# Kernel optimization log

Hardware: AMD Instinct MI355X
Metric: run time of the kernel (lower is better)

The kernel has to match this reference:

```python
import jax, jax.numpy as jnp
import numpy as np

B, S, D, DH, H, HD, F, L = 32, 4096, 256, 128, 8, 32, 64, 4
EPS_BN, EPS_LN = 1e-5, 1e-5


def _conv1d(x, w, b, pad):
    # x: [B,C,S], w: [O,I,K] (torch layout)
    y = jax.lax.conv_general_dilated(x, w, (1,), [(pad, pad)],
                                     dimension_numbers=('NCH', 'OIH', 'NCH'))
    return y + b[None, :, None]


def _bn_eval(x, g, b):
    # BatchNorm1d in eval mode with running_mean=0, running_var=1 (fresh init)
    return x * (g / jnp.sqrt(1.0 + EPS_BN))[None, :, None] + b[None, :, None]


def _ln(x, g, b):
    m = x.mean(-1, keepdims=True)
    v = ((x - m) ** 2).mean(-1, keepdims=True)
    return (x - m) / jnp.sqrt(v + EPS_LN) * g + b


def _gelu(x):
    return jax.nn.gelu(x, approximate=False)


def _pos_encoding(seq_len, d_model):
    pos = jnp.arange(seq_len, dtype=jnp.float32)[:, None]
    div = jnp.exp(jnp.arange(0, d_model, 2, dtype=jnp.float32) * (-np.log(10000.0) / d_model))
    pe = jnp.zeros((seq_len, d_model), jnp.float32)
    pe = pe.at[:, 0::2].set(jnp.sin(pos * div))
    pe = pe.at[:, 1::2].set(jnp.cos(pos * div))
    return pe


def _performer_attn(x, wq, bq, wk, bk, wv, bv, wo, bo, rf):
    b_, s_, d_ = x.shape
    def heads(y):
        return y.reshape(b_, s_, H, HD).transpose(0, 2, 1, 3)  # [B,H,S,hd]
    q, k, v = heads(x @ wq + bq), heads(x @ wk + bk), heads(x @ wv + bv)
    qp = jax.nn.softplus(jnp.einsum('bhsd,hdf->bhsf', q, rf))
    kp = jax.nn.softplus(jnp.einsum('bhsd,hdf->bhsf', k, rf))
    kv = jnp.einsum('bhsf,bhsd->bhfd', kp, v)          # [B,H,F,hd]
    ksum = kp.sum(axis=2)                              # [B,H,F]
    qkv = jnp.einsum('bhsf,bhfd->bhsd', qp, kv)
    denom = jnp.einsum('bhsf,bhf->bhs', qp, ksum) + 1e-8
    out = (qkv / denom[..., None]).transpose(0, 2, 1, 3).reshape(b_, s_, d_)
    return out @ wo + bo


def _forward(x, emb_w1, emb_b1, bn1_g, bn1_b, emb_w2, emb_b2, bn2_g, bn2_b,
             wq, bq, wk, bk, wv, bv, wo, bo, rf,
             ln1_g, ln1_b, ln2_g, ln2_b, ff_w1, ff_b1, ff_w2, ff_b2,
             dec_w1, dec_b1, bn3_g, bn3_b, dec_w2, dec_b2):
    h = _gelu(_bn_eval(_conv1d(x[:, None, :], emb_w1, emb_b1, 3), bn1_g, bn1_b))
    h = _gelu(_bn_eval(_conv1d(h, emb_w2, emb_b2, 2), bn2_g, bn2_b))
    h = h.transpose(0, 2, 1)                           # [B,S,D]
    h = h + _pos_encoding(h.shape[1], h.shape[2])[None]
    for i in range(L):
        a = _performer_attn(_ln(h, ln1_g[i], ln1_b[i]),
                            wq[i], bq[i], wk[i], bk[i], wv[i], bv[i], wo[i], bo[i], rf[i])
        h = h + a
        f = _ln(h, ln2_g[i], ln2_b[i])
        f = _gelu(f @ ff_w1[i] + ff_b1[i]) @ ff_w2[i] + ff_b2[i]
        h = h + f
    hc = h.transpose(0, 2, 1)
    hc = _gelu(_bn_eval(_conv1d(hc, dec_w1, dec_b1, 2), bn3_g, bn3_b))
    hc = _conv1d(hc, dec_w2, dec_b2, 1)
    return jax.nn.sigmoid(hc)[:, 0, :]                 # [B,S]


def setup_inputs() -> dict:
    key = jax.random.key(0)
    ks = iter(jax.random.split(key, 64))
    def rn(shape, s=1.0):
        return jax.random.normal(next(ks), shape, jnp.float32) * s
    return {
        'x': rn((B, S)),
        'emb_w1': rn((DH, 1, 7), 0.3), 'emb_b1': rn((DH,), 0.02),
        'bn1_g': 1.0 + rn((DH,), 0.02), 'bn1_b': rn((DH,), 0.02),
        'emb_w2': rn((D, DH, 5), 0.05), 'emb_b2': rn((D,), 0.02),
        'bn2_g': 1.0 + rn((D,), 0.02), 'bn2_b': rn((D,), 0.02),
        'wq': rn((L, D, D), 0.05), 'bq': rn((L, D), 0.02),
        'wk': rn((L, D, D), 0.05), 'bk': rn((L, D), 0.02),
        'wv': rn((L, D, D), 0.05), 'bv': rn((L, D), 0.02),
        'wo': rn((L, D, D), 0.05), 'bo': rn((L, D), 0.02),
        'rf': rn((L, H, HD, F), 1.0 / np.sqrt(F)),
        'ln1_g': jnp.ones((L, D)), 'ln1_b': jnp.zeros((L, D)),
        'ln2_g': jnp.ones((L, D)), 'ln2_b': jnp.zeros((L, D)),
        'ff_w1': rn((L, D, 4 * D), 0.05), 'ff_b1': rn((L, 4 * D), 0.02),
        'ff_w2': rn((L, 4 * D, D), 0.03), 'ff_b2': rn((L, D), 0.02),
        'dec_w1': rn((DH, D, 5), 0.05), 'dec_b1': rn((DH,), 0.02),
        'bn3_g': 1.0 + rn((DH,), 0.02), 'bn3_b': rn((DH,), 0.02),
        'dec_w2': rn((1, DH, 3), 0.1), 'dec_b2': rn((1,), 0.02),
    }


def reference(x, emb_w1, emb_b1, bn1_g, bn1_b, emb_w2, emb_b2, bn2_g, bn2_b,
              wq, bq, wk, bk, wv, bv, wo, bo, rf,
              ln1_g, ln1_b, ln2_g, ln2_b, ff_w1, ff_b1, ff_w2, ff_b2,
              dec_w1, dec_b1, bn3_g, bn3_b, dec_w2, dec_b2):
    return _forward(x, emb_w1, emb_b1, bn1_g, bn1_b, emb_w2, emb_b2, bn2_g, bn2_b,
                    wq, bq, wk, bk, wv, bv, wo, bo, rf,
                    ln1_g, ln1_b, ln2_g, ln2_b, ff_w1, ff_b1, ff_w2, ff_b2,
                    dec_w1, dec_b1, bn3_g, bn3_b, dec_w2, dec_b2)
```

## Files before the change

kernel.cpp:

```cpp
#include <hip/hip_runtime.h>
#include <hip/hip_bf16.h>
#include <math.h>


typedef __bf16 bf16_t;
typedef __bf16 bf16x8 __attribute__((ext_vector_type(8)));
typedef __bf16 bf16x4 __attribute__((ext_vector_type(4)));
typedef float  f32x4  __attribute__((ext_vector_type(4)));

#define DEV __device__ __forceinline__

DEV float erf_fast(float x) {
  float ax = fabsf(x);
  float t = __builtin_amdgcn_rcpf(1.f + 0.3275911f * ax);
  float p = t * (0.254829592f + t * (-0.284496736f + t * (1.421413741f +
            t * (-1.453152027f + t * 1.061405429f))));
  float r = 1.f - p * __expf(-ax * ax);
  return copysignf(r, x);
}
DEV float geluf(float v) { return 0.5f * v * (1.f + erf_fast(v * 0.70710678118654752440f)); }
DEV float softplusf(float v) {
  float e = __expf(-fabsf(v));
  return fmaxf(v, 0.f) + __logf(1.f + e);
}

DEV void gload16(const bf16_t* g, bf16_t* l) {
  __builtin_amdgcn_global_load_lds(
      (const __attribute__((address_space(1))) void*)g,
      (__attribute__((address_space(3))) void*)l, 16, 0, 0);
}

template <int EPI, int K>
__global__ __launch_bounds__(256, 3)
void gemm_bf16(const bf16_t* __restrict__ A, const bf16_t* __restrict__ Bt,
               void* Cout, const float* __restrict__ bias,
               const float* __restrict__ scale, const float* resid,
               const float* __restrict__ pe,
               int lda, long a_bstride, int rpb,
               int N, int ldc, long c_bstride, int c_roff)
{
  __shared__ bf16_t As[3][128 * 32];
  __shared__ bf16_t Bs[3][128 * 32];
  const int t = threadIdx.x;
  const int lane = t & 63;
  const int w = t >> 6;
  const int wm = w >> 1, wn = w & 1;
  const long m0 = (long)blockIdx.x * 128;
  const int n0 = blockIdx.y * 128;
  const int b = (int)(m0 / rpb);
  const int s_base = (int)(m0 % rpb);
  const bf16_t* Ab = A + (long)b * a_bstride + (long)s_base * lda;
  const bf16_t* Bb = Bt + (long)n0 * K;

  const int srow = lane >> 2;
  const int sslot = (lane & 3) ^ ((srow >> 1) & 3);
  const bf16_t* aS = Ab + (long)(w * 32 + srow) * lda + sslot * 8;
  const bf16_t* bS = Bb + (long)(w * 32 + srow) * K + sslot * 8;
  const int dsto = w * 1024;

#define STAGE(bufidx, kk)                                   \
  {                                                         \
    bf16_t* a_ = &As[bufidx][dsto];                         \
    bf16_t* b_ = &Bs[bufidx][dsto];                         \
    gload16(aS + (kk), a_);                                 \
    gload16(aS + (kk) + 16 * (long)lda, a_ + 512);          \
    gload16(bS + (kk), b_);                                 \
    gload16(bS + (kk) + 16 * (long)K, b_ + 512);            \
  }

  f32x4 acc[4][4];
#pragma unroll
  for (int i = 0; i < 4; i++)
#pragma unroll
    for (int j = 0; j < 4; j++) acc[i][j] = (f32x4){0.f, 0.f, 0.f, 0.f};

  constexpr int NT = K >> 5;
  STAGE(0, 0);
  STAGE(1, 32);

#pragma unroll
  for (int tt = 0; tt < NT; ++tt) {
    if (tt + 1 < NT) {
      asm volatile("s_waitcnt vmcnt(4)" ::: "memory");
    } else {
      asm volatile("s_waitcnt vmcnt(0)" ::: "memory");
    }
    __builtin_amdgcn_s_barrier();
    __builtin_amdgcn_sched_barrier(0);
    if (tt + 2 < NT) STAGE((tt + 2) % 3, (tt + 2) * 32);
    const int cb = tt % 3;
    const bf16_t* Acur = As[cb];
    const bf16_t* Bcur = Bs[cb];
    const int kb = (lane >> 4) * 16;
    bf16x8 af[4], bfr[4];
#pragma unroll
    for (int i = 0; i < 4; i++) {
      int rA = wm * 64 + i * 16 + (lane & 15);
      af[i] = *(const bf16x8*)((const char*)Acur + rA * 64 + (kb ^ (((rA >> 1) & 3) << 4)));
      int rB = wn * 64 + i * 16 + (lane & 15);
      bfr[i] = *(const bf16x8*)((const char*)Bcur + rB * 64 + (kb ^ (((rB >> 1) & 3) << 4)));
    }
    __builtin_amdgcn_s_setprio(1);
#pragma unroll
    for (int mi = 0; mi < 4; mi++)
#pragma unroll
      for (int ni = 0; ni < 4; ni++)
        acc[mi][ni] = __builtin_amdgcn_mfma_f32_16x16x32_bf16(af[mi], bfr[ni], acc[mi][ni], 0, 0, 0);
    __builtin_amdgcn_s_setprio(0);
  }
#undef STAGE

  const int colbase = n0 + wn * 64 + (lane & 15);
  float bias_r[4], scale_r[4];
#pragma unroll
  for (int ni = 0; ni < 4; ni++) {
    int col = colbase + ni * 16;
    bias_r[ni] = bias[col];
    scale_r[ni] = (EPI == 3 || EPI == 4) ? scale[col] : 0.f;
  }
#pragma unroll
  for (int mi = 0; mi < 4; mi++) {
#pragma unroll
    for (int j = 0; j < 4; j++) {
      int row = wm * 64 + mi * 16 + ((lane >> 4) << 2) + j;
      long s = s_base + row;
      long cro = (long)b * c_bstride + (s + c_roff) * (long)ldc;
#pragma unroll
      for (int ni = 0; ni < 4; ni++) {
        int col = colbase + ni * 16;
        float v = acc[mi][ni][j];
        if constexpr (EPI == 1) {
          v += bias_r[ni] + resid[cro + col];
          ((float*)Cout)[cro + col] = v;
        } else if constexpr (EPI == 2) {
          v = geluf(v + bias_r[ni]);
          ((bf16_t*)Cout)[cro + col] = (bf16_t)v;
        } else if constexpr (EPI == 3) {
          v = geluf(v * scale_r[ni] + bias_r[ni]) + pe[s * 256 + col];
          ((float*)Cout)[cro + col] = v;
        } else if constexpr (EPI == 4) {
          v = geluf(v * scale_r[ni] + bias_r[ni]);
          ((bf16_t*)Cout)[cro + col] = (bf16_t)v;
        } else {
          v += bias_r[ni];
          if (col < 1024) v = softplusf(v);
          ((bf16_t*)Cout)[cro + col] = (bf16_t)v;
        }
      }
    }
  }
}

__global__ __launch_bounds__(256)
void ln_kernel(const float* __restrict__ h, const float* __restrict__ g,
               const float* __restrict__ bta, bf16_t* __restrict__ out)
{
  int t = threadIdx.x;
  int lane = t & 63;
  long row = (long)blockIdx.x * 4 + (t >> 6);
  const float* hp = h + row * 256 + lane * 4;
  float4 v = *(const float4*)hp;
  float s = v.x + v.y + v.z + v.w;
  float q = v.x * v.x + v.y * v.y + v.z * v.z + v.w * v.w;
#pragma unroll
  for (int m = 32; m >= 1; m >>= 1) {
    s += __shfl_xor(s, m);
    q += __shfl_xor(q, m);
  }
  float mean = s * 0.00390625f;
  float var = q * 0.00390625f - mean * mean;
  float rstd = rsqrtf(var + 1e-5f);
  int c = lane * 4;
  float4 gv = *(const float4*)(g + c);
  float4 bv = *(const float4*)(bta + c);
  bf16x4 o;
  o[0] = (bf16_t)((v.x - mean) * rstd * gv.x + bv.x);
  o[1] = (bf16_t)((v.y - mean) * rstd * gv.y + bv.y);
  o[2] = (bf16_t)((v.z - mean) * rstd * gv.z + bv.z);
  o[3] = (bf16_t)((v.w - mean) * rstd * gv.w + bv.w);
  *(bf16x4*)(out + row * 256 + c) = o;
}

__global__ __launch_bounds__(256)
void conv1_kernel(const float* __restrict__ x, const float* __restrict__ w1,
                  const float* __restrict__ sc, const float* __restrict__ sb,
                  bf16_t* __restrict__ h1p)
{
  int b = blockIdx.x >> 6;
  int s0 = (blockIdx.x & 63) << 6;
  __shared__ float xs[70];
  __shared__ float ws[896];
  int t = threadIdx.x;
  if (t < 70) {
    int s = s0 + t - 3;
    xs[t] = (s >= 0 && s < 4096) ? x[(long)b * 4096 + s] : 0.f;
  }
  for (int i = t; i < 896; i += 256) ws[i] = w1[i];
  __syncthreads();
  int c = t & 127, so = t >> 7;
  float wr[7];
#pragma unroll
  for (int k = 0; k < 7; k++) wr[k] = ws[c * 7 + k];
  float scl = sc[c], sbv = sb[c];
  for (int p = 0; p < 32; p++) {
    int sl = p * 2 + so;
    float a = 0.f;
#pragma unroll
    for (int k = 0; k < 7; k++) a += xs[sl + k] * wr[k];
    a = geluf(a * scl + sbv);
    h1p[((long)b * 4100 + s0 + sl + 2) * 128 + c] = (bf16_t)a;
  }
}

__global__ __launch_bounds__(256)
void kv_partial(const bf16_t* __restrict__ qpkpv,
                float* __restrict__ pkv, float* __restrict__ pks)
{
  int bh = blockIdx.x >> 3, ch = blockIdx.x & 7;
  int b = bh >> 3, hh = bh & 7;
  int s0 = ch * 512;
  __shared__ float kps[32 * 64];
  __shared__ float vs[32 * 32];
  int t = threadIdx.x;
  int f = t & 63, dg = t >> 6;
  float acc[8] = {0.f, 0.f, 0.f, 0.f, 0.f, 0.f, 0.f, 0.f};
  float ks = 0.f;
  const int row = t >> 3, slot8 = (t & 7) * 8, slot4 = (t & 7) * 4;
  for (int sb = 0; sb < 512; sb += 32) {
    __syncthreads();
    {
      const bf16_t* rowp = qpkpv + ((long)b * 4096 + s0 + sb + row) * 1280;
      bf16x8 k8 = *(const bf16x8*)(rowp + 512 + hh * 64 + slot8);
#pragma unroll
      for (int j = 0; j < 8; j++) kps[row * 64 + slot8 + j] = (float)k8[j];
      bf16x4 v4 = *(const bf16x4*)(rowp + 1024 + hh * 32 + slot4);
#pragma unroll
      for (int j = 0; j < 4; j++) vs[row * 32 + slot4 + j] = (float)v4[j];
    }
    __syncthreads();
#pragma unroll 4
    for (int s = 0; s < 32; s++) {
      float kval = kps[s * 64 + f];
      float4 v0 = *(const float4*)&vs[s * 32 + dg * 8];
      float4 v1 = *(const float4*)&vs[s * 32 + dg * 8 + 4];
      acc[0] += kval * v0.x; acc[1] += kval * v0.y;
      acc[2] += kval * v0.z; acc[3] += kval * v0.w;
      acc[4] += kval * v1.x; acc[5] += kval * v1.y;
      acc[6] += kval * v1.z; acc[7] += kval * v1.w;
      ks += kval;
    }
  }
  long o = (long)blockIdx.x * 2048 + f * 32 + dg * 8;
#pragma unroll
  for (int j = 0; j < 8; j++) pkv[o + j] = acc[j];
  if (dg == 0) pks[blockIdx.x * 64 + f] = ks;
}

__global__ __launch_bounds__(256)
void kv_reduce(const float* __restrict__ pkv, const float* __restrict__ pks,
               float* __restrict__ kv, float* __restrict__ ksum, int nbh)
{
  long idx = (long)blockIdx.x * 256 + threadIdx.x;
  {
    int bh = (int)(idx >> 11), fd = (int)(idx & 2047);
    float s = 0.f;
#pragma unroll
    for (int ch = 0; ch < 8; ch++) s += pkv[((long)(bh * 8 + ch)) * 2048 + fd];
    kv[idx] = s;
  }
  if (idx < (long)nbh * 64) {
    int bh = (int)(idx >> 6), f = (int)(idx & 63);
    float s = 0.f;
#pragma unroll
    for (int ch = 0; ch < 8; ch++) s += pks[(bh * 8 + ch) * 64 + f];
    ksum[idx] = s;
  }
}

__global__ __launch_bounds__(256, 2)
void combine_mfma(const bf16_t* __restrict__ qpkpv, const float* __restrict__ kv,
                  const float* __restrict__ ksum, bf16_t* __restrict__ ao)
{
  int bh = blockIdx.x >> 5;
  int s0 = (blockIdx.x & 31) << 7;
  int b = bh >> 3, hh = bh & 7;
  __shared__ bf16_t A_s[128 * 72];
  __shared__ bf16_t B_s[48 * 72];
  int t = threadIdx.x;
  for (int g = t; g < 1024; g += 256) {
    int row = g >> 3, slot = (g & 7) * 8;
    *(bf16x8*)&A_s[row * 72 + slot] =
        *(const bf16x8*)(qpkpv + ((long)b * 4096 + s0 + row) * 1280 + hh * 64 + slot);
  }
  for (int i = t; i < 2048; i += 256) {
    int f = i >> 5, d = i & 31;
    B_s[d * 72 + f] = (bf16_t)kv[(long)bh * 2048 + i];
  }
  if (t < 64) B_s[32 * 72 + t] = (bf16_t)ksum[bh * 64 + t];
  for (int i = t; i < 960; i += 256) {
    int n = 33 + (i >> 6), f = i & 63;
    B_s[n * 72 + f] = (bf16_t)0.f;
  }
  __syncthreads();
  int lane = t & 63, w = t >> 6;
  f32x4 acc[2][3];
#pragma unroll
  for (int i = 0; i < 2; i++)
#pragma unroll
    for (int j = 0; j < 3; j++) acc[i][j] = (f32x4){0.f, 0.f, 0.f, 0.f};
#pragma unroll
  for (int kt = 0; kt < 2; kt++) {
    int ko = kt * 32 + (lane >> 4) * 8;
    bf16x8 a[2], bb[3];
#pragma unroll
    for (int i = 0; i < 2; i++)
      a[i] = *(const bf16x8*)&A_s[(w * 32 + i * 16 + (lane & 15)) * 72 + ko];
#pragma unroll
    for (int i = 0; i < 3; i++)
      bb[i] = *(const bf16x8*)&B_s[(i * 16 + (lane & 15)) * 72 + ko];
#pragma unroll
    for (int mi = 0; mi < 2; mi++)
#pragma unroll
      for (int ni = 0; ni < 3; ni++)
        acc[mi][ni] = __builtin_amdgcn_mfma_f32_16x16x32_bf16(a[mi], bb[ni], acc[mi][ni], 0, 0, 0);
  }
  long sbase = (long)b * 4096 + s0;
#pragma unroll
  for (int mi = 0; mi < 2; mi++)
#pragma unroll
    for (int j = 0; j < 4; j++) {
      int r = w * 32 + mi * 16 + ((lane >> 4) << 2) + j;
      float den = __shfl(acc[mi][2][j], (lane & 48)) + 1e-8f;
#pragma unroll
      for (int ni = 0; ni < 2; ni++) {
        int d = ni * 16 + (lane & 15);
        ao[(sbase + r) * 256 + hh * 32 + d] = (bf16_t)(acc[mi][ni][j] / den);
      }
    }
}

__global__ __launch_bounds__(256)
void cast_pad(const float* __restrict__ h, bf16_t* __restrict__ hp)
{
  long i8 = ((long)blockIdx.x * 256 + threadIdx.x) * 8;
  long r = i8 >> 8;
  int c = (int)(i8 & 255);
  int b = (int)(r >> 12), s = (int)(r & 4095);
  float4 v0 = *(const float4*)(h + i8);
  float4 v1 = *(const float4*)(h + i8 + 4);
  bf16x8 o;
  o[0] = (bf16_t)v0.x; o[1] = (bf16_t)v0.y; o[2] = (bf16_t)v0.z; o[3] = (bf16_t)v0.w;
  o[4] = (bf16_t)v1.x; o[5] = (bf16_t)v1.y; o[6] = (bf16_t)v1.z; o[7] = (bf16_t)v1.w;
  *(bf16x8*)(hp + ((long)b * 4100 + s + 2) * 256 + c) = o;
}

__global__ __launch_bounds__(256)
void conv_final(const bf16_t* __restrict__ hdp, const float* __restrict__ w2,
                const float* __restrict__ b2, float* __restrict__ out)
{
  __shared__ float ws[384];
  int t = threadIdx.x;
  for (int i = t; i < 384; i += 256) ws[i] = w2[i];
  __syncthreads();
  long idx = (long)blockIdx.x * 256 + t;
  int b = (int)(idx >> 12);
  const bf16_t* base = hdp + ((long)b * 4098 + (idx & 4095)) * 128;
  float a = b2[0];
#pragma unroll
  for (int k = 0; k < 3; k++) {
#pragma unroll
    for (int c8 = 0; c8 < 16; c8++) {
      bf16x8 v = *(const bf16x8*)(base + k * 128 + c8 * 8);
#pragma unroll
      for (int j = 0; j < 8; j++) a += (float)v[j] * ws[(c8 * 8 + j) * 3 + k];
    }
  }
  out[idx] = 1.f / (1.f + __expf(-a));
}

__global__ __launch_bounds__(256)
void prep_weff(const float* __restrict__ wq, const float* __restrict__ wk,
               const float* __restrict__ wv, const float* __restrict__ bq,
               const float* __restrict__ bk, const float* __restrict__ bv,
               const float* __restrict__ rf, bf16_t* __restrict__ weff,
               float* __restrict__ beff)
{
  long idx = (long)blockIdx.x * 256 + threadIdx.x;
  int d = (int)(idx & 255);
  long r = idx >> 8;
  int n = (int)(r % 1280);
  int l = (int)(r / 1280);
  float val;
  if (n < 1024) {
    int qk = n >> 9;
    int h = (n >> 6) & 7;
    int f = n & 63;
    const float* w = qk ? wk : wq;
    const float* rfh = rf + ((long)(l * 8 + h) * 32) * 64 + f;
    const float* wrow = w + ((long)l * 256 + d) * 256 + h * 32;
    float s = 0.f;
#pragma unroll
    for (int hd = 0; hd < 32; hd++) s += wrow[hd] * rfh[hd * 64];
    val = s;
  } else {
    val = wv[((long)l * 256 + d) * 256 + (n - 1024)];
  }
  weff[idx] = (bf16_t)val;
  if (idx < 4 * 1280) {
    int nn = (int)(idx % 1280);
    int ll = (int)(idx / 1280);
    float bvv;
    if (nn < 1024) {
      int qk = nn >> 9;
      int h = (nn >> 6) & 7;
      int f = nn & 63;
      const float* bsrc = qk ? bk : bq;
      float s = 0.f;
      for (int hd = 0; hd < 32; hd++)
        s += bsrc[ll * 256 + h * 32 + hd] * rf[((long)(ll * 8 + h) * 32 + hd) * 64 + f];
      bvv = s;
    } else {
      bvv = bv[ll * 256 + (nn - 1024)];
    }
    beff[idx] = bvv;
  }
}

__global__ __launch_bounds__(256)
void prep_cast_t(const float* __restrict__ src, bf16_t* __restrict__ dst, int K, int N)
{
  long idx = (long)blockIdx.x * 256 + threadIdx.x;
  int k = (int)(idx % K);
  long r = idx / K;
  int n = (int)(r % N);
  int l = (int)(r / N);
  dst[idx] = (bf16_t)src[((long)l * K + k) * N + n];
}

__global__ __launch_bounds__(256)
void prep_conv_t(const float* __restrict__ w, bf16_t* __restrict__ dst, int C, int KW)
{
  long idx = (long)blockIdx.x * 256 + threadIdx.x;
  int ckw = C * KW;
  int kk = (int)(idx % ckw);
  int o = (int)(idx / ckw);
  int kw = kk / C, c = kk % C;
  dst[idx] = (bf16_t)w[((long)o * C + c) * KW + kw];
}

__global__ __launch_bounds__(256)
void prep_bn(const float* g1, const float* b1, const float* cb1,
             const float* g2, const float* b2, const float* cb2,
             const float* g3, const float* b3, const float* cb3,
             float* sc1, float* sb1, float* sc2, float* sb2,
             float* sc3, float* sb3)
{
  int t = threadIdx.x;
  const float r = rsqrtf(1.f + 1e-5f);
  if (t < 128) { float s = g1[t] * r; sc1[t] = s; sb1[t] = cb1[t] * s + b1[t]; }
  if (t < 256) { float s = g2[t] * r; sc2[t] = s; sb2[t] = cb2[t] * s + b2[t]; }
  if (t < 128) { float s = g3[t] * r; sc3[t] = s; sb3[t] = cb3[t] * s + b3[t]; }
}

__global__ __launch_bounds__(256)
void pe_fill(float* __restrict__ pe)
{
  long idx = (long)blockIdx.x * 256 + threadIdx.x;
  int dcol = (int)(idx & 255);
  int s = (int)(idx >> 8);
  int i2 = dcol >> 1;
  float freq = expf(-9.210340371976184f * (float)(2 * i2) / 256.f);
  float a = (float)s * freq;
  pe[idx] = (dcol & 1) ? cosf(a) : sinf(a);
}

extern "C" void kernel_launch(void* const* d_in, const int* in_sizes, int n_in,
                              void* d_out, int out_size, void* d_ws, size_t ws_size,
                              hipStream_t stream)
{
  (void)in_sizes; (void)n_in; (void)out_size;
  const float* x      = (const float*)d_in[0];
  const float* emb_w1 = (const float*)d_in[1];
  const float* emb_b1 = (const float*)d_in[2];
  const float* bn1_g  = (const float*)d_in[3];
  const float* bn1_b  = (const float*)d_in[4];
  const float* emb_w2 = (const float*)d_in[5];
  const float* emb_b2 = (const float*)d_in[6];
  const float* bn2_g  = (const float*)d_in[7];
  const float* bn2_b  = (const float*)d_in[8];
  const float* wq     = (const float*)d_in[9];
  const float* bq     = (const float*)d_in[10];
  const float* wk     = (const float*)d_in[11];
  const float* bk     = (const float*)d_in[12];
  const float* wv     = (const float*)d_in[13];
  const float* bv     = (const float*)d_in[14];
  const float* wo     = (const float*)d_in[15];
  const float* bo     = (const float*)d_in[16];
  const float* rf     = (const float*)d_in[17];
  const float* ln1_g  = (const float*)d_in[18];
  const float* ln1_b  = (const float*)d_in[19];
  const float* ln2_g  = (const float*)d_in[20];
  const float* ln2_b  = (const float*)d_in[21];
  const float* ff_w1  = (const float*)d_in[22];
  const float* ff_b1  = (const float*)d_in[23];
  const float* ff_w2  = (const float*)d_in[24];
  const float* ff_b2  = (const float*)d_in[25];
  const float* dec_w1 = (const float*)d_in[26];
  const float* dec_b1 = (const float*)d_in[27];
  const float* bn3_g  = (const float*)d_in[28];
  const float* bn3_b  = (const float*)d_in[29];
  const float* dec_w2 = (const float*)d_in[30];
  const float* dec_b2 = (const float*)d_in[31];

  char* W = (char*)d_ws;

  bf16_t* weff = (bf16_t*)(W + 0);
  float*  beff = (float*)(W + 2621440);
  bf16_t* wot  = (bf16_t*)(W + 2641920);
  bf16_t* w1t  = (bf16_t*)(W + 3166208);
  bf16_t* w2t  = (bf16_t*)(W + 5263360);
  bf16_t* c2t  = (bf16_t*)(W + 7360512);
  bf16_t* d1t  = (bf16_t*)(W + 7688192);
  float*  pe   = (float*)(W + 8015872);
  float*  sc1  = (float*)(W + 12210176);
  float*  sb1  = (float*)(W + 12211200);
  float*  sc2  = (float*)(W + 12212224);
  float*  sb2  = (float*)(W + 12213248);
  float*  sc3  = (float*)(W + 12214272);
  float*  sb3  = (float*)(W + 12215296);
  const size_t FIXED_END = 16777216;

  const size_t PER_B = 17385472;
  int Bc = 32;
  while (Bc > 1 && FIXED_END + (size_t)Bc * PER_B > ws_size) Bc >>= 1;

  char* P = W + FIXED_END;
  float*  h     = (float*)P;
  bf16_t* xa    = (bf16_t*)(P + (size_t)Bc * 4194304);
  bf16_t* ao    = xa;
  char*   big   = P + (size_t)Bc * (4194304 + 2097152);
  bf16_t* qpkpv = (bf16_t*)big;
  bf16_t* f1    = (bf16_t*)big;
  bf16_t* h1p   = (bf16_t*)big;
  bf16_t* hpad  = (bf16_t*)big;
  bf16_t* hdp   = (bf16_t*)(big + (size_t)Bc * 4100 * 256 * 2);
  float*  pkv   = (float*)(big + (size_t)Bc * 10485760);
  float*  pks   = (float*)((char*)pkv + (size_t)Bc * 524288);
  float*  kvb   = (float*)((char*)pks + (size_t)Bc * 16384);
  float*  ksum  = (float*)((char*)kvb + (size_t)Bc * 65536);

  prep_weff<<<5120, 256, 0, stream>>>(wq, wk, wv, bq, bk, bv, rf, weff, beff);
  prep_cast_t<<<1024, 256, 0, stream>>>(wo, wot, 256, 256);
  prep_cast_t<<<4096, 256, 0, stream>>>(ff_w1, w1t, 256, 1024);
  prep_cast_t<<<4096, 256, 0, stream>>>(ff_w2, w2t, 1024, 256);
  prep_conv_t<<<640, 256, 0, stream>>>(emb_w2, c2t, 128, 5);
  prep_conv_t<<<640, 256, 0, stream>>>(dec_w1, d1t, 256, 5);
  prep_bn<<<1, 256, 0, stream>>>(bn1_g, bn1_b, emb_b1, bn2_g, bn2_b, emb_b2,
                                 bn3_g, bn3_b, dec_b1, sc1, sb1, sc2, sb2, sc3, sb3);
  pe_fill<<<4096, 256, 0, stream>>>(pe);

  for (int c0 = 0; c0 < 32; c0 += Bc) {
    const float* xc = x + (size_t)c0 * 4096;

    hipMemsetAsync(h1p, 0, (size_t)Bc * 4100 * 128 * 2, stream);
    conv1_kernel<<<Bc * 64, 256, 0, stream>>>(xc, emb_w1, sc1, sb1, h1p);
    gemm_bf16<3, 640><<<dim3(Bc * 32, 2), 256, 0, stream>>>(
        h1p, c2t, h, sb2, sc2, nullptr, pe,
        128, 4100L * 128, 4096, 256, 256, 4096L * 256, 0);

    for (int l = 0; l < 4; l++) {
      ln_kernel<<<Bc * 1024, 256, 0, stream>>>(h, ln1_g + l * 256, ln1_b + l * 256, xa);
      gemm_bf16<5, 256><<<dim3(Bc * 32, 10), 256, 0, stream>>>(
          xa, weff + (long)l * 327680, qpkpv, beff + l * 1280, nullptr, nullptr, nullptr,
          256, 4096L * 256, 4096, 1280, 1280, 4096L * 1280, 0);
      kv_partial<<<Bc * 64, 256, 0, stream>>>(qpkpv, pkv, pks);
      kv_reduce<<<Bc * 64, 256, 0, stream>>>(pkv, pks, kvb, ksum, Bc * 8);
      combine_mfma<<<Bc * 256, 256, 0, stream>>>(qpkpv, kvb, ksum, ao);
      gemm_bf16<1, 256><<<dim3(Bc * 32, 2), 256, 0, stream>>>(
          ao, wot + (long)l * 65536, h, bo + l * 256, nullptr, h, nullptr,
          256, 4096L * 256, 4096, 256, 256, 4096L * 256, 0);
      ln_kernel<<<Bc * 1024, 256, 0, stream>>>(h, ln2_g + l * 256, ln2_b + l * 256, xa);
      gemm_bf16<2, 256><<<dim3(Bc * 32, 8), 256, 0, stream>>>(
          xa, w1t + (long)l * 262144, f1, ff_b1 + l * 1024, nullptr, nullptr, nullptr,
          256, 4096L * 256, 4096, 1024, 1024, 4096L * 1024, 0);
      gemm_bf16<1, 1024><<<dim3(Bc * 32, 2), 256, 0, stream>>>(
          f1, w2t + (long)l * 262144, h, ff_b2 + l * 256, nullptr, h, nullptr,
          1024, 4096L * 1024, 4096, 256, 256, 4096L * 256, 0);
    }

    hipMemsetAsync(hpad, 0, (size_t)Bc * 4100 * 256 * 2, stream);
    cast_pad<<<Bc * 512, 256, 0, stream>>>(h, hpad);
    hipMemsetAsync(hdp, 0, (size_t)Bc * 4098 * 128 * 2, stream);
    gemm_bf16<4, 1280><<<dim3(Bc * 32, 1), 256, 0, stream>>>(
        hpad, d1t, hdp, sb3, sc3, nullptr, nullptr,
        256, 4100L * 256, 4096, 128, 128, 4098L * 128, 1);
    conv_final<<<Bc * 16, 256, 0, stream>>>(hdp, dec_w2, dec_b2,
                                            (float*)d_out + (size_t)c0 * 4096);
  }
}
```

Before: 4.479 ms.

## Deepen GEMM LDS pipeline to four stages and fold kv_reduce into combine

The bf16 GEMM moves from triple to quadruple LDS buffering, with one more tile prefetched ahead and adjusted vmcnt waits. Its occupancy hint drops from 3 to 2 blocks per CU to make room for the extra shared memory. Separately, the kv_reduce kernel is removed: each combine_mfma block now sums the 8 partial kv/ksum chunks itself while filling its B tile. This saves a launch and an intermediate buffer per layer, but the reduction is now repeated by all 32 sequence blocks of each head.

```diff
diff --git a/kernel.cpp b/kernel.cpp
--- a/kernel.cpp
+++ b/kernel.cpp
@@ -31,7 +31,7 @@
 }
 
 template <int EPI, int K>
-__global__ __launch_bounds__(256, 3)
+__global__ __launch_bounds__(256, 2)
 void gemm_bf16(const bf16_t* __restrict__ A, const bf16_t* __restrict__ Bt,
                void* Cout, const float* __restrict__ bias,
                const float* __restrict__ scale, const float* resid,
@@ -39,8 +39,8 @@
                int lda, long a_bstride, int rpb,
                int N, int ldc, long c_bstride, int c_roff)
 {
-  __shared__ bf16_t As[3][128 * 32];
-  __shared__ bf16_t Bs[3][128 * 32];
+  __shared__ bf16_t As[4][128 * 32];
+  __shared__ bf16_t Bs[4][128 * 32];
   const int t = threadIdx.x;
   const int lane = t & 63;
   const int w = t >> 6;
@@ -77,18 +77,21 @@
   constexpr int NT = K >> 5;
   STAGE(0, 0);
   STAGE(1, 32);
+  STAGE(2, 64);
 
 #pragma unroll
   for (int tt = 0; tt < NT; ++tt) {
-    if (tt + 1 < NT) {
+    if (tt + 2 < NT) {
+      asm volatile("s_waitcnt vmcnt(8)" ::: "memory");
+    } else if (tt + 1 < NT) {
       asm volatile("s_waitcnt vmcnt(4)" ::: "memory");
     } else {
       asm volatile("s_waitcnt vmcnt(0)" ::: "memory");
     }
     __builtin_amdgcn_s_barrier();
     __builtin_amdgcn_sched_barrier(0);
-    if (tt + 2 < NT) STAGE((tt + 2) % 3, (tt + 2) * 32);
-    const int cb = tt % 3;
+    if (tt + 3 < NT) STAGE((tt + 3) & 3, (tt + 3) * 32);
+    const int cb = tt & 3;
     const bf16_t* Acur = As[cb];
     const bf16_t* Bcur = Bs[cb];
     const int kb = (lane >> 4) * 16;
@@ -256,30 +259,9 @@
   if (dg == 0) pks[blockIdx.x * 64 + f] = ks;
 }
 
-__global__ __launch_bounds__(256)
-void kv_reduce(const float* __restrict__ pkv, const float* __restrict__ pks,
-               float* __restrict__ kv, float* __restrict__ ksum, int nbh)
-{
-  long idx = (long)blockIdx.x * 256 + threadIdx.x;
-  {
-    int bh = (int)(idx >> 11), fd = (int)(idx & 2047);
-    float s = 0.f;
-#pragma unroll
-    for (int ch = 0; ch < 8; ch++) s += pkv[((long)(bh * 8 + ch)) * 2048 + fd];
-    kv[idx] = s;
-  }
-  if (idx < (long)nbh * 64) {
-    int bh = (int)(idx >> 6), f = (int)(idx & 63);
-    float s = 0.f;
-#pragma unroll
-    for (int ch = 0; ch < 8; ch++) s += pks[(bh * 8 + ch) * 64 + f];
-    ksum[idx] = s;
-  }
-}
-
 __global__ __launch_bounds__(256, 2)
-void combine_mfma(const bf16_t* __restrict__ qpkpv, const float* __restrict__ kv,
-                  const float* __restrict__ ksum, bf16_t* __restrict__ ao)
+void combine_mfma(const bf16_t* __restrict__ qpkpv, const float* __restrict__ pkv,
+                  const float* __restrict__ pks, bf16_t* __restrict__ ao)
 {
   int bh = blockIdx.x >> 5;
   int s0 = (blockIdx.x & 31) << 7;
@@ -293,10 +275,18 @@
         *(const bf16x8*)(qpkpv + ((long)b * 4096 + s0 + row) * 1280 + hh * 64 + slot);
   }
   for (int i = t; i < 2048; i += 256) {
+    float s = 0.f;
+#pragma unroll
+    for (int ch = 0; ch < 8; ch++) s += pkv[((long)(bh * 8 + ch)) * 2048 + i];
     int f = i >> 5, d = i & 31;
-    B_s[d * 72 + f] = (bf16_t)kv[(long)bh * 2048 + i];
-  }
-  if (t < 64) B_s[32 * 72 + t] = (bf16_t)ksum[bh * 64 + t];
+    B_s[d * 72 + f] = (bf16_t)s;
+  }
+  if (t < 64) {
+    float s = 0.f;
+#pragma unroll
+    for (int ch = 0; ch < 8; ch++) s += pks[(bh * 8 + ch) * 64 + t];
+    B_s[32 * 72 + t] = (bf16_t)s;
+  }
   for (int i = t; i < 960; i += 256) {
     int n = 33 + (i >> 6), f = i & 63;
     B_s[n * 72 + f] = (bf16_t)0.f;
@@ -546,8 +536,6 @@
   bf16_t* hdp   = (bf16_t*)(big + (size_t)Bc * 4100 * 256 * 2);
   float*  pkv   = (float*)(big + (size_t)Bc * 10485760);
   float*  pks   = (float*)((char*)pkv + (size_t)Bc * 524288);
-  float*  kvb   = (float*)((char*)pks + (size_t)Bc * 16384);
-  float*  ksum  = (float*)((char*)kvb + (size_t)Bc * 65536);
 
   prep_weff<<<5120, 256, 0, stream>>>(wq, wk, wv, bq, bk, bv, rf, weff, beff);
   prep_cast_t<<<1024, 256, 0, stream>>>(wo, wot, 256, 256);
@@ -574,8 +562,7 @@
           xa, weff + (long)l * 327680, qpkpv, beff + l * 1280, nullptr, nullptr, nullptr,
           256, 4096L * 256, 4096, 1280, 1280, 4096L * 1280, 0);
       kv_partial<<<Bc * 64, 256, 0, stream>>>(qpkpv, pkv, pks);
-      kv_reduce<<<Bc * 64, 256, 0, stream>>>(pkv, pks, kvb, ksum, Bc * 8);
-      combine_mfma<<<Bc * 256, 256, 0, stream>>>(qpkpv, kvb, ksum, ao);
+      combine_mfma<<<Bc * 256, 256, 0, stream>>>(qpkpv, pkv, pks, ao);
       gemm_bf16<1, 256><<<dim3(Bc * 32, 2), 256, 0, stream>>>(
           ao, wot + (long)l * 65536, h, bo + l * 256, nullptr, h, nullptr,
           256, 4096L * 256, 4096, 256, 256, 4096L * 256, 0);
```

Result: slower. 4.940 ms (+10.3%).
